# Kernel optimization log

Hardware: AMD Instinct MI355X
Metric: run time of the kernel (lower is better)

The kernel has to match this reference:

```python
import jax, jax.numpy as jnp
import numpy as np

N_NODES = 100000
N_EDGES = 1600000
HIDDEN = 128
EF_DIM = 16
LAYERS = 2
N_GRAPHS = 64


def _residual(x, W, b):
    # Residual(mlp_num=2): x + act(act(x@W0+b0)@W1+b1), act = silu
    h = jax.nn.silu(x @ W[0] + b[0])
    h = jax.nn.silu(h @ W[1] + b[1])
    return x + h


def setup_inputs() -> dict:
    key = jax.random.key(0)
    ks = jax.random.split(key, 10)
    scalar = jax.random.normal(ks[0], (N_NODES, HIDDEN), jnp.float32)
    ef = jax.random.normal(ks[1], (N_EDGES, EF_DIM), jnp.float32)
    edge_index = jax.random.randint(ks[2], (2, N_EDGES), 0, N_NODES, jnp.int32)
    C = jax.random.uniform(ks[3], (N_NODES, 1), dtype=jnp.float32)
    conv_smooth = jax.random.uniform(ks[4], (N_EDGES, 1), dtype=jnp.float32)
    batch_index = jnp.sort(jax.random.randint(ks[5], (N_NODES,), 0, N_GRAPHS, jnp.int32))
    # per VD_Conv layer: emb0, emb1, conv0, conv1, out0, out1 residual blocks; + 3 pooling blocks
    n_res = LAYERS * 6 + 3
    res_W = jax.random.normal(ks[6], (n_res, 2, HIDDEN, HIDDEN), jnp.float32) * 0.02
    res_b = jnp.zeros((n_res, 2, HIDDEN), jnp.float32)
    e_lin = jax.random.normal(ks[7], (LAYERS, EF_DIM, HIDDEN), jnp.float32) * 0.02
    return {"scalar": scalar, "ef": ef, "edge_index": edge_index, "C": C,
            "conv_smooth": conv_smooth, "batch_index": batch_index,
            "res_W": res_W, "res_b": res_b, "e_lin": e_lin}


def reference(scalar, ef, edge_index, C, conv_smooth, batch_index, res_W, res_b, e_lin):
    row, col = edge_index[0], edge_index[1]
    for i in range(LAYERS):
        p = 6 * i
        s_src = _residual(scalar, res_W[p], res_b[p])
        s_dst = _residual(scalar, res_W[p + 1], res_b[p + 1])
        conv_filter = (ef @ e_lin[i]) * conv_smooth            # [E, H]
        scalar_edge = s_dst[col] * conv_filter                 # gather + elementwise filter
        conv = jax.ops.segment_sum(scalar_edge, row, num_segments=N_NODES) * C  # scatter-reduce (agg='sum')
        conv = _residual(_residual(conv, res_W[p + 2], res_b[p + 2]), res_W[p + 3], res_b[p + 3])
        s = s_src * conv
        s = _residual(_residual(s, res_W[p + 4], res_b[p + 4]), res_W[p + 5], res_b[p + 5])
        scalar = s + scalar                                    # outer residual in Vanilla_DisGNN
    graph = jax.ops.segment_sum(scalar, batch_index, num_segments=N_GRAPHS)
    q = 6 * LAYERS
    for j in range(3):
        graph = _residual(graph, res_W[q + j], res_b[q + j])
    return graph
```

## Files before the change

### kernel.cpp

```cpp
#include <hip/hip_runtime.h>
#include <hip/hip_bf16.h>
#include <cstdint>
#include <cstddef>

#define HD 128
#define WOFF 16384

typedef __bf16    bf16x8 __attribute__((ext_vector_type(8)));
typedef float     f32x4  __attribute__((ext_vector_type(4)));
typedef _Float16  h2     __attribute__((ext_vector_type(2)));
typedef _Float16  h8     __attribute__((ext_vector_type(8)));

#if defined(__has_builtin)
#if __has_builtin(__builtin_amdgcn_fdot2)
#define HAVE_FDOT2 1
#endif
#endif

__device__ __forceinline__ float fdot2f(h2 a, h2 b, float c) {
#ifdef HAVE_FDOT2
    return __builtin_amdgcn_fdot2(a, b, c, false);
#else
    return c + (float)a[0]*(float)b[0] + (float)a[1]*(float)b[1];
#endif
}

__device__ __forceinline__ int swz(int r, int byteInRow) {
    int chunk = (byteInRow >> 4) ^ (r & 7);
    return r * 256 + (chunk << 4) + (byteInRow & 15);
}

__device__ __forceinline__ float silu_f(float v) { return v / (1.f + __expf(-v)); }


__device__ __forceinline__ void stage_x64(const float* __restrict__ x, char* lds,
                                          int r0, int nrows, int tid) {
    const int q = tid & 15;
    #pragma unroll
    for (int rr = 0; rr < 2; ++rr) {
        const int r  = (tid >> 4) + rr * 32;
        const int gr = r0 + r;
        float4 a = {0,0,0,0}, b = {0,0,0,0};
        if (gr < nrows) {
            const float4* p = (const float4*)(x + (size_t)gr * HD + q * 8);
            a = p[0]; b = p[1];
        }
        bf16x8 v;
        v[0]=(__bf16)a.x; v[1]=(__bf16)a.y; v[2]=(__bf16)a.z; v[3]=(__bf16)a.w;
        v[4]=(__bf16)b.x; v[5]=(__bf16)b.y; v[6]=(__bf16)b.z; v[7]=(__bf16)b.w;
        *(bf16x8*)(lds + swz(r, q * 16)) = v;
    }
}

__device__ __forceinline__ void load_wpref(const __bf16* __restrict__ w, bf16x8 pref[4], int tid) {
    #pragma unroll
    for (int i = 0; i < 4; ++i)
        pref[i] = *(const bf16x8*)(w + (size_t)(i * 512 + tid) * 8);
}
__device__ __forceinline__ void store_wpref(char* lds, const bf16x8 pref[4], int tid) {
    #pragma unroll
    for (int i = 0; i < 4; ++i) {
        const int l = i * 512 + tid;
        *(bf16x8*)(lds + WOFF + swz(l >> 4, (l & 15) * 16)) = pref[i];
    }
}

__device__ __forceinline__ void mm_pass_lds(const char* lds,
                                            const float* __restrict__ bias,
                                            int mrow0, int nbase, int crow, int kgrp, f32x4 acc[4]) {
    bf16x8 afr[4];
    #pragma unroll
    for (int kk = 0; kk < 4; ++kk)
        afr[kk] = *(const bf16x8*)(lds + swz(mrow0 + crow, kk*64 + kgrp*16));
    #pragma unroll
    for (int ni = 0; ni < 4; ++ni) {
        const float bv = bias[(nbase + ni) * 16 + crow];
        f32x4 t = {bv, bv, bv, bv};
        acc[ni] = t;
    }
    #pragma unroll
    for (int ni = 0; ni < 4; ++ni) {
        #pragma unroll
        for (int kk = 0; kk < 4; ++kk) {
            const bf16x8 bfr = *(const bf16x8*)(lds + WOFF + swz((nbase+ni)*16 + crow, kk*64 + kgrp*16));
            acc[ni] = __builtin_amdgcn_mfma_f32_16x16x32_bf16(afr[kk], bfr, acc[ni], 0, 0, 0);
        }
    }
}

__device__ __forceinline__ void write_h64(char* lds, const f32x4 acc[4],
                                          int mrow0, int nbase, int crow, int kgrp) {
    #pragma unroll
    for (int ni = 0; ni < 4; ++ni)
        #pragma unroll
        for (int rg = 0; rg < 4; ++rg)
            *(__bf16*)(lds + swz(mrow0 + kgrp*4 + rg, ((nbase+ni)*16 + crow)*2)) =
                (__bf16)silu_f(acc[ni][rg]);
}

__device__ __forceinline__ void restage64(char* lds, const f32x4 carry[4],
                                          int mrow0, int nbase, int crow, int kgrp) {
    #pragma unroll
    for (int ni = 0; ni < 4; ++ni)
        #pragma unroll
        for (int rg = 0; rg < 4; ++rg)
            *(__bf16*)(lds + swz(mrow0 + kgrp*4 + rg, ((nbase+ni)*16 + crow)*2)) =
                (__bf16)carry[ni][rg];
}

__global__ __launch_bounds__(512) void resid_dual_kernel(
    const float* __restrict__ x,
    const __bf16* __restrict__ wtA, const float* __restrict__ bA,
    const __bf16* __restrict__ wtB, const float* __restrict__ bB,
    __bf16* __restrict__ out1, __bf16* __restrict__ out2, int nrows)
{
    __shared__ char lds[49152];
    const int tid = threadIdx.x, lane = tid & 63, wv = tid >> 6;
    const int crow = lane & 15, kgrp = lane >> 4;
    const int r0 = blockIdx.x * 64;
    const int mrow0 = (wv >> 1) * 16, nbase = (wv & 1) * 4;

    {
        bf16x8 pref[4];
        load_wpref(wtA, pref, tid);
        stage_x64(x, lds, r0, nrows, tid);
        store_wpref(lds, pref, tid);
    }
    f32x4 acc[4], xe[4];
    #pragma unroll
    for (int ni = 0; ni < 4; ++ni)
        #pragma unroll
        for (int rg = 0; rg < 4; ++rg) {
            const int gr = r0 + mrow0 + kgrp*4 + rg;
            xe[ni][rg] = (gr < nrows) ? x[(size_t)gr*HD + (nbase+ni)*16 + crow] : 0.f;
        }
    __syncthreads();

    {
        bf16x8 pref[4];
        load_wpref(wtA + 16384, pref, tid);
        mm_pass_lds(lds, bA, mrow0, nbase, crow, kgrp, acc);
        __syncthreads();
        write_h64(lds, acc, mrow0, nbase, crow, kgrp);
        store_wpref(lds, pref, tid);
        __syncthreads();
    }
    {
        bf16x8 pref[4];
        load_wpref(wtB, pref, tid);
        mm_pass_lds(lds, bA + HD, mrow0, nbase, crow, kgrp, acc);
        #pragma unroll
        for (int ni = 0; ni < 4; ++ni)
            #pragma unroll
            for (int rg = 0; rg < 4; ++rg) {
                const int gr = r0 + mrow0 + kgrp*4 + rg;
                if (gr < nrows)
                    out1[(size_t)gr*HD + (nbase+ni)*16 + crow] =
                        (__bf16)(xe[ni][rg] + silu_f(acc[ni][rg]));
            }
        __syncthreads();
        restage64(lds, xe, mrow0, nbase, crow, kgrp);
        store_wpref(lds, pref, tid);
        __syncthreads();
    }
    {
        bf16x8 pref[4];
        load_wpref(wtB + 16384, pref, tid);
        mm_pass_lds(lds, bB, mrow0, nbase, crow, kgrp, acc);
        __syncthreads();
        write_h64(lds, acc, mrow0, nbase, crow, kgrp);
        store_wpref(lds, pref, tid);
        __syncthreads();
    }
    mm_pass_lds(lds, bB + HD, mrow0, nbase, crow, kgrp, acc);
    #pragma unroll
    for (int ni = 0; ni < 4; ++ni)
        #pragma unroll
        for (int rg = 0; rg < 4; ++rg) {
            const int gr = r0 + mrow0 + kgrp*4 + rg;
            if (gr < nrows)
                out2[(size_t)gr*HD + (nbase+ni)*16 + crow] =
                    (__bf16)(xe[ni][rg] + silu_f(acc[ni][rg]));
        }
}

__device__ __forceinline__ void sub_block(char* lds, const __bf16* __restrict__ w1,
                                          const __bf16* __restrict__ wNext0,
                                          const float* __restrict__ bias,
                                          int tid, int mrow0, int nbase, int crow, int kgrp,
                                          f32x4 carry[4], f32x4 acc[4]) {
    {
        bf16x8 pref[4];
        load_wpref(w1, pref, tid);
        mm_pass_lds(lds, bias, mrow0, nbase, crow, kgrp, acc);
        __syncthreads();
        write_h64(lds, acc, mrow0, nbase, crow, kgrp);
        store_wpref(lds, pref, tid);
        __syncthreads();
    }
    {
        bf16x8 pref[4];
        load_wpref(wNext0, pref, tid);
        mm_pass_lds(lds, bias + HD, mrow0, nbase, crow, kgrp, acc);
        #pragma unroll
        for (int ni = 0; ni < 4; ++ni)
            #pragma unroll
            for (int rg = 0; rg < 4; ++rg) carry[ni][rg] += silu_f(acc[ni][rg]);
        __syncthreads();
        restage64(lds, carry, mrow0, nbase, crow, kgrp);
        store_wpref(lds, pref, tid);
        __syncthreads();
    }
}

__global__ __launch_bounds__(512) void chain4_kernel(
    const float* __restrict__ x, const __bf16* __restrict__ mid,
    const __bf16* __restrict__ wA, const float* __restrict__ bA,
    const __bf16* __restrict__ wB, const float* __restrict__ bB,
    const __bf16* __restrict__ wC, const float* __restrict__ bC,
    const __bf16* __restrict__ wD, const float* __restrict__ bD,
    const float* __restrict__ post, float* __restrict__ y, int nrows)
{
    __shared__ char lds[49152];
    const int tid = threadIdx.x, lane = tid & 63, wv = tid >> 6;
    const int crow = lane & 15, kgrp = lane >> 4;
    const int r0 = blockIdx.x * 64;
    const int mrow0 = (wv >> 1) * 16, nbase = (wv & 1) * 4;

    {
        bf16x8 pref[4];
        load_wpref(wA, pref, tid);
        stage_x64(x, lds, r0, nrows, tid);
        store_wpref(lds, pref, tid);
    }
    f32x4 carry[4], acc[4];
    #pragma unroll
    for (int ni = 0; ni < 4; ++ni)
        #pragma unroll
        for (int rg = 0; rg < 4; ++rg) {
            const int gr = r0 + mrow0 + kgrp*4 + rg;
            carry[ni][rg] = (gr < nrows) ? x[(size_t)gr*HD + (nbase+ni)*16 + crow] : 0.f;
        }
    __syncthreads();

    sub_block(lds, wA + 16384, wB, bA, tid, mrow0, nbase, crow, kgrp, carry, acc);
    {
        bf16x8 pref[4];
        load_wpref(wB + 16384, pref, tid);
        mm_pass_lds(lds, bB, mrow0, nbase, crow, kgrp, acc);
        __syncthreads();
        write_h64(lds, acc, mrow0, nbase, crow, kgrp);
        store_wpref(lds, pref, tid);
        __syncthreads();
    }
    {
        bf16x8 pref[4];
        load_wpref(wC, pref, tid);
        mm_pass_lds(lds, bB + HD, mrow0, nbase, crow, kgrp, acc);
        #pragma unroll
        for (int ni = 0; ni < 4; ++ni)
            #pragma unroll
            for (int rg = 0; rg < 4; ++rg) {
                const int gr = r0 + mrow0 + kgrp*4 + rg;
                const float m = (gr < nrows) ? (float)mid[(size_t)gr*HD + (nbase+ni)*16 + crow] : 0.f;
                carry[ni][rg] = (carry[ni][rg] + silu_f(acc[ni][rg])) * m;
            }
        __syncthreads();
        restage64(lds, carry, mrow0, nbase, crow, kgrp);
        store_wpref(lds, pref, tid);
        __syncthreads();
    }
    sub_block(lds, wC + 16384, wD, bC, tid, mrow0, nbase, crow, kgrp, carry, acc);
    {
        bf16x8 pref[4];
        load_wpref(wD + 16384, pref, tid);
        mm_pass_lds(lds, bD, mrow0, nbase, crow, kgrp, acc);
        __syncthreads();
        write_h64(lds, acc, mrow0, nbase, crow, kgrp);
        store_wpref(lds, pref, tid);
        __syncthreads();
    }
    mm_pass_lds(lds, bD + HD, mrow0, nbase, crow, kgrp, acc);
    #pragma unroll
    for (int ni = 0; ni < 4; ++ni)
        #pragma unroll
        for (int rg = 0; rg < 4; ++rg) {
            const int gr = r0 + mrow0 + kgrp*4 + rg;
            if (gr < nrows) {
                const int cc = (nbase+ni)*16 + crow;
                y[(size_t)gr*HD + cc] = carry[ni][rg] + silu_f(acc[ni][rg]) + post[(size_t)gr*HD + cc];
            }
        }
}

__global__ __launch_bounds__(512) void chain3_kernel(
    const float* __restrict__ x,
    const __bf16* __restrict__ wA, const float* __restrict__ bA,
    const __bf16* __restrict__ wB, const float* __restrict__ bB,
    const __bf16* __restrict__ wC, const float* __restrict__ bC,
    float* __restrict__ y, int nrows)
{
    __shared__ char lds[49152];
    const int tid = threadIdx.x, lane = tid & 63, wv = tid >> 6;
    const int crow = lane & 15, kgrp = lane >> 4;
    const int r0 = blockIdx.x * 64;
    const int mrow0 = (wv >> 1) * 16, nbase = (wv & 1) * 4;

    {
        bf16x8 pref[4];
        load_wpref(wA, pref, tid);
        stage_x64(x, lds, r0, nrows, tid);
        store_wpref(lds, pref, tid);
    }
    f32x4 carry[4], acc[4];
    #pragma unroll
    for (int ni = 0; ni < 4; ++ni)
        #pragma unroll
        for (int rg = 0; rg < 4; ++rg) {
            const int gr = r0 + mrow0 + kgrp*4 + rg;
            carry[ni][rg] = (gr < nrows) ? x[(size_t)gr*HD + (nbase+ni)*16 + crow] : 0.f;
        }
    __syncthreads();

    sub_block(lds, wA + 16384, wB, bA, tid, mrow0, nbase, crow, kgrp, carry, acc);
    sub_block(lds, wB + 16384, wC, bB, tid, mrow0, nbase, crow, kgrp, carry, acc);
    {
        bf16x8 pref[4];
        load_wpref(wC + 16384, pref, tid);
        mm_pass_lds(lds, bC, mrow0, nbase, crow, kgrp, acc);
        __syncthreads();
        write_h64(lds, acc, mrow0, nbase, crow, kgrp);
        store_wpref(lds, pref, tid);
        __syncthreads();
    }
    mm_pass_lds(lds, bC + HD, mrow0, nbase, crow, kgrp, acc);
    #pragma unroll
    for (int ni = 0; ni < 4; ++ni)
        #pragma unroll
        for (int rg = 0; rg < 4; ++rg) {
            const int gr = r0 + mrow0 + kgrp*4 + rg;
            if (gr < nrows)
                y[(size_t)gr*HD + (nbase+ni)*16 + crow] = carry[ni][rg] + silu_f(acc[ni][rg]);
        }
}

__global__ __launch_bounds__(256) void hist_kernel(const int* __restrict__ erow, int* __restrict__ cnt, int E) {
    int i = blockIdx.x * blockDim.x + threadIdx.x;
    const int stride = gridDim.x * blockDim.x;
    for (; i < E; i += stride) atomicAdd(&cnt[erow[i]], 1);
}

__global__ __launch_bounds__(256) void scan1_kernel(const int* __restrict__ cnt, int* __restrict__ part, int n) {
    __shared__ int red[256];
    const int base = blockIdx.x * 1024;
    int s = 0;
    for (int i = threadIdx.x; i < 1024; i += 256) {
        const int idx = base + i;
        s += (idx < n) ? cnt[idx] : 0;
    }
    red[threadIdx.x] = s; __syncthreads();
    for (int o = 128; o > 0; o >>= 1) {
        if (threadIdx.x < o) red[threadIdx.x] += red[threadIdx.x + o];
        __syncthreads();
    }
    if (threadIdx.x == 0) part[blockIdx.x] = red[0];
}

__global__ __launch_bounds__(256) void scan2_kernel(int* __restrict__ part, int nb,
                                                    int* __restrict__ rowptr, int n) {
    __shared__ int sh[257];
    const int tid = threadIdx.x;
    int a[4]; int s = 0;
    #pragma unroll
    for (int q = 0; q < 4; ++q) {
        const int i = tid*4 + q;
        a[q] = (i < nb) ? part[i] : 0;
        s += a[q];
    }
    sh[tid + 1] = s; __syncthreads();
    if (tid == 0) {
        sh[0] = 0;
        int run = 0;
        for (int i = 1; i <= 256; ++i) { run += sh[i]; sh[i] = run; }
    }
    __syncthreads();
    int off = sh[tid];
    #pragma unroll
    for (int q = 0; q < 4; ++q) {
        const int i = tid*4 + q;
        if (i < nb) part[i] = off;
        off += a[q];
    }
    if (tid == 255) rowptr[n] = off;
}

__global__ __launch_bounds__(256) void scan3_kernel(const int* __restrict__ cnt, const int* __restrict__ part,
                                                    int* __restrict__ rowptr, int n) {
    __shared__ int sc[257];
    const int base = blockIdx.x * 1024;
    const int i0 = base + threadIdx.x * 4;
    int v[4]; int s = 0;
    #pragma unroll
    for (int q = 0; q < 4; ++q) {
        const int idx = i0 + q;
        v[q] = (idx < n) ? cnt[idx] : 0;
        s += v[q];
    }
    sc[threadIdx.x + 1] = s; __syncthreads();
    if (threadIdx.x == 0) {
        int run = 0;
        for (int i = 0; i < 256; ++i) { const int t = sc[i + 1]; sc[i + 1] = run; run += t; }
    }
    __syncthreads();
    int off = part[blockIdx.x] + sc[threadIdx.x + 1];
    #pragma unroll
    for (int q = 0; q < 4; ++q) {
        const int idx = i0 + q;
        if (idx < n) rowptr[idx] = off;
        off += v[q];
    }
}

__global__ __launch_bounds__(256) void scatter_reorder_kernel(
    const int* __restrict__ erow, const int* __restrict__ ecol,
    const float* __restrict__ ef, const float* __restrict__ cs,
    const int* __restrict__ rowptr, int* __restrict__ cursor,
    int* __restrict__ csr_col, _Float16* __restrict__ csr_ef, int E)
{
    int i = blockIdx.x * blockDim.x + threadIdx.x;
    const int stride = gridDim.x * blockDim.x;
    for (; i < E; i += stride) {
        const int r = erow[i];
        const int p = rowptr[r] + atomicAdd(&cursor[r], 1);
        csr_col[p] = ecol[i];
        const float c = cs[i];
        const float4* ep = (const float4*)(ef + (size_t)i * 16);
        const float4 e0 = ep[0], e1 = ep[1], e2 = ep[2], e3 = ep[3];
        h8 v0, v1;
        v0[0]=(_Float16)(e0.x*c); v0[1]=(_Float16)(e0.y*c); v0[2]=(_Float16)(e0.z*c); v0[3]=(_Float16)(e0.w*c);
        v0[4]=(_Float16)(e1.x*c); v0[5]=(_Float16)(e1.y*c); v0[6]=(_Float16)(e1.z*c); v0[7]=(_Float16)(e1.w*c);
        v1[0]=(_Float16)(e2.x*c); v1[1]=(_Float16)(e2.y*c); v1[2]=(_Float16)(e2.z*c); v1[3]=(_Float16)(e2.w*c);
        v1[4]=(_Float16)(e3.x*c); v1[5]=(_Float16)(e3.y*c); v1[6]=(_Float16)(e3.z*c); v1[7]=(_Float16)(e3.w*c);
        h8* dst = (h8*)(csr_ef + (size_t)p * 16);
        dst[0] = v0; dst[1] = v1;
    }
}

__global__ __launch_bounds__(256) void elin16_kernel(const float* __restrict__ elin,
                                                     _Float16* __restrict__ out, int total) {
    const int i = blockIdx.x * 256 + threadIdx.x;
    if (i < total) out[i] = (_Float16)elin[i];
}

__device__ __forceinline__ float bfu_lo(uint32_t u) { return __uint_as_float(u << 16); }
__device__ __forceinline__ float bfu_hi(uint32_t u) { return __uint_as_float(u & 0xffff0000u); }

__device__ __forceinline__ void edge_dot(const h8 a0, const h8 a1,
                                         const h2 w0[8], const h2 w1[8],
                                         float& f0, float& f1) {
    #pragma unroll
    for (int kk = 0; kk < 4; ++kk) {
        h2 p = {a0[2*kk], a0[2*kk+1]};
        f0 = fdot2f(p, w0[kk], f0);
        f1 = fdot2f(p, w1[kk], f1);
    }
    #pragma unroll
    for (int kk = 0; kk < 4; ++kk) {
        h2 p = {a1[2*kk], a1[2*kk+1]};
        f0 = fdot2f(p, w0[4+kk], f0);
        f1 = fdot2f(p, w1[4+kk], f1);
    }
}

__global__ __launch_bounds__(256) void conv_kernel(
    const _Float16* __restrict__ csr_ef, const int* __restrict__ csr_col,
    const _Float16* __restrict__ elin16, const int* __restrict__ rowptr,
    const __bf16* __restrict__ sdst, const float* __restrict__ Cn,
    float* __restrict__ conv, int nnodes)
{
    const int wv   = __builtin_amdgcn_readfirstlane(threadIdx.x >> 6);
    const int lane = threadIdx.x & 63;
    const int v = blockIdx.x * 4 + wv;
    if (v >= nnodes) return;
    const int j0 = lane * 2;

    h2 w0[8], w1[8];
    #pragma unroll
    for (int kk = 0; kk < 8; ++kk) {
        w0[kk][0] = elin16[(2*kk)   * HD + j0];
        w0[kk][1] = elin16[(2*kk+1) * HD + j0];
        w1[kk][0] = elin16[(2*kk)   * HD + j0 + 1];
        w1[kk][1] = elin16[(2*kk+1) * HD + j0 + 1];
    }

    const uint16_t* sd = (const uint16_t*)sdst;
    const int beg = rowptr[v], end = rowptr[v + 1];
    float acc0 = 0.f, acc1 = 0.f;
    int t = beg;
    for (; t + 8 <= end; t += 8) {
        int c[8];
        #pragma unroll
        for (int q = 0; q < 8; ++q) c[q] = csr_col[t + q];
        uint32_t u[8];
        #pragma unroll
        for (int q = 0; q < 8; ++q)
            u[q] = *(const uint32_t*)(sd + (size_t)c[q] * HD + j0);
        #pragma unroll
        for (int q = 0; q < 8; ++q) {
            const h8* ep = (const h8*)(csr_ef + (size_t)(t + q) * 16);
            const h8 a0 = ep[0], a1 = ep[1];
            float f0 = 0.f, f1 = 0.f;
            edge_dot(a0, a1, w0, w1, f0, f1);
            acc0 = fmaf(bfu_lo(u[q]), f0, acc0);
            acc1 = fmaf(bfu_hi(u[q]), f1, acc1);
        }
    }
    for (; t + 2 <= end; t += 2) {
        int c[2];
        c[0] = csr_col[t]; c[1] = csr_col[t + 1];
        uint32_t u[2];
        u[0] = *(const uint32_t*)(sd + (size_t)c[0] * HD + j0);
        u[1] = *(const uint32_t*)(sd + (size_t)c[1] * HD + j0);
        #pragma unroll
        for (int q = 0; q < 2; ++q) {
            const h8* ep = (const h8*)(csr_ef + (size_t)(t + q) * 16);
            const h8 a0 = ep[0], a1 = ep[1];
            float f0 = 0.f, f1 = 0.f;
            edge_dot(a0, a1, w0, w1, f0, f1);
            acc0 = fmaf(bfu_lo(u[q]), f0, acc0);
            acc1 = fmaf(bfu_hi(u[q]), f1, acc1);
        }
    }
    if (t < end) {
        const int c = csr_col[t];
        const uint32_t u = *(const uint32_t*)(sd + (size_t)c * HD + j0);
        const h8* ep = (const h8*)(csr_ef + (size_t)t * 16);
        const h8 a0 = ep[0], a1 = ep[1];
        float f0 = 0.f, f1 = 0.f;
        edge_dot(a0, a1, w0, w1, f0, f1);
        acc0 = fmaf(bfu_lo(u), f0, acc0);
        acc1 = fmaf(bfu_hi(u), f1, acc1);
    }
    const float cn = Cn[v];
    float2 out = {acc0 * cn, acc1 * cn};
    *(float2*)(conv + (size_t)v * HD + j0) = out;
}

__global__ __launch_bounds__(256) void pool_kernel(
    const float* __restrict__ s, const int* __restrict__ bidx,
    float* __restrict__ g, int n)
{
    const int slot = threadIdx.x >> 5;
    const int jc   = (threadIdx.x & 31) * 4;
    const int base = blockIdx.x * 256;
    if (base >= n) return;
    const int end = (base + 256 < n) ? base + 256 : n;
    float4 acc = {0,0,0,0};
    int cur = -1;
    for (int i = base + slot; i < end; i += 8) {
        const int b = bidx[i];
        if (b != cur) {
            if (cur >= 0) {
                atomicAdd(g + (size_t)cur*HD + jc + 0, acc.x);
                atomicAdd(g + (size_t)cur*HD + jc + 1, acc.y);
                atomicAdd(g + (size_t)cur*HD + jc + 2, acc.z);
                atomicAdd(g + (size_t)cur*HD + jc + 3, acc.w);
            }
            acc = {0,0,0,0};
            cur = b;
        }
        const float4 v = *(const float4*)(s + (size_t)i*HD + jc);
        acc.x += v.x; acc.y += v.y; acc.z += v.z; acc.w += v.w;
    }
    if (cur >= 0) {
        atomicAdd(g + (size_t)cur*HD + jc + 0, acc.x);
        atomicAdd(g + (size_t)cur*HD + jc + 1, acc.y);
        atomicAdd(g + (size_t)cur*HD + jc + 2, acc.z);
        atomicAdd(g + (size_t)cur*HD + jc + 3, acc.w);
    }
}

__global__ __launch_bounds__(256) void convw_kernel(const float* __restrict__ W, __bf16* __restrict__ wt, int total) {
    const int idx = blockIdx.x * 256 + threadIdx.x;
    if (idx >= total) return;
    const int mat = idx >> 14;
    const int rem = idx & 16383;
    const int jj = rem >> 7, kk = rem & 127;
    wt[idx] = (__bf16)W[(size_t)mat * 16384 + kk * HD + jj];
}

extern "C" void kernel_launch(void* const* d_in, const int* in_sizes, int n_in,
                              void* d_out, int out_size, void* d_ws, size_t ws_size,
                              hipStream_t stream) {
    const float* scalar = (const float*)d_in[0];
    const float* ef     = (const float*)d_in[1];
    const int*   eidx   = (const int*)  d_in[2];
    const float* Cn     = (const float*)d_in[3];
    const float* cs     = (const float*)d_in[4];
    const int*   bidx   = (const int*)  d_in[5];
    const float* resW   = (const float*)d_in[6];
    const float* resB   = (const float*)d_in[7];
    const float* elin   = (const float*)d_in[8];

    const int N      = in_sizes[0] / HD;
    const int E      = in_sizes[1] / 16;
    const int n_res  = in_sizes[7] / (2 * HD);
    const int layers = (n_res - 3) / 6;
    const int G      = out_size / HD;
    const size_t nfeat = (size_t)N * HD;

    char* p = (char*)d_ws;
    auto alloc = [&](size_t bytes) { char* q = p; p += (bytes + 255) & ~(size_t)255; return q; };
    float*    A      = (float*)alloc(nfeat * 4);
    float*    Dc     = (float*)alloc(nfeat * 4);
    __bf16*   Bs16   = (__bf16*)alloc(nfeat * 2);
    __bf16*   Cs16   = (__bf16*)alloc(nfeat * 2);
    __bf16*   wt     = (__bf16*)alloc((size_t)n_res * 2 * 16384 * 2);
    float*    graph  = (float*)alloc((size_t)G * HD * 4);
    int*      rowptr = (int*)alloc((size_t)(N + 1) * 4);
    int*      rowcnt = (int*)alloc((size_t)N * 4);
    int*      csr_col= (int*)alloc((size_t)E * 4);
    _Float16* csr_ef = (_Float16*)alloc((size_t)E * 16 * 2);
    _Float16* elin16 = (_Float16*)alloc((size_t)layers * 16 * HD * 2);
    int*      part   = (int*)alloc(1024 * 4);

    const int* erow = eidx;
    const int* ecol = eidx + E;

    const int totW = n_res * 2 * 16384;
    convw_kernel<<<(totW + 255) / 256, 256, 0, stream>>>(resW, wt, totW);
    const int totE = layers * 16 * HD;
    elin16_kernel<<<(totE + 255) / 256, 256, 0, stream>>>(elin, elin16, totE);

    const int nchunks = (N + 1023) / 1024;
    hipMemsetAsync(rowcnt, 0, (size_t)N * 4, stream);
    hist_kernel<<<1024, 256, 0, stream>>>(erow, rowcnt, E);
    scan1_kernel<<<nchunks, 256, 0, stream>>>(rowcnt, part, N);
    scan2_kernel<<<1, 256, 0, stream>>>(part, nchunks, rowptr, N);
    scan3_kernel<<<nchunks, 256, 0, stream>>>(rowcnt, part, rowptr, N);
    hipMemsetAsync(rowcnt, 0, (size_t)N * 4, stream);
    scatter_reorder_kernel<<<1024, 256, 0, stream>>>(erow, ecol, ef, cs, rowptr, rowcnt, csr_col, csr_ef, E);

    const int gridR = (N + 63) / 64;
    const float* cur = scalar;
    for (int i = 0; i < layers; ++i) {
        const int pb = 6 * i;
        resid_dual_kernel<<<gridR, 512, 0, stream>>>(
            cur,
            wt + (size_t)pb * 32768, resB + (size_t)pb * 256,
            wt + (size_t)(pb + 1) * 32768, resB + (size_t)(pb + 1) * 256,
            Bs16, Cs16, N);
        conv_kernel<<<(N + 3) / 4, 256, 0, stream>>>(
            csr_ef, csr_col, elin16 + (size_t)i * 16 * HD, rowptr, Cs16, Cn, Dc, N);
        chain4_kernel<<<gridR, 512, 0, stream>>>(
            Dc, Bs16,
            wt + (size_t)(pb + 2) * 32768, resB + (size_t)(pb + 2) * 256,
            wt + (size_t)(pb + 3) * 32768, resB + (size_t)(pb + 3) * 256,
            wt + (size_t)(pb + 4) * 32768, resB + (size_t)(pb + 4) * 256,
            wt + (size_t)(pb + 5) * 32768, resB + (size_t)(pb + 5) * 256,
            cur, A, N);
        cur = A;
    }

    hipMemsetAsync(graph, 0, (size_t)G * HD * 4, stream);
    pool_kernel<<<(N + 255) / 256, 256, 0, stream>>>(cur, bidx, graph, N);

    const int q = 6 * layers;
    const int gridG = (G + 63) / 64;
    chain3_kernel<<<gridG, 512, 0, stream>>>(
        graph,
        wt + (size_t)q * 32768, resB + (size_t)q * 256,
        wt + (size_t)(q + 1) * 32768, resB + (size_t)(q + 1) * 256,
        wt + (size_t)(q + 2) * 32768, resB + (size_t)(q + 2) * 256,
        (float*)d_out, G);
}
```

Measured before the change: 840.9 us.

## Switch residual MLP kernels to 32x32 MFMA tiles with direct global-to-LDS weight staging

```diff
diff --git a/kernel.cpp b/kernel.cpp
--- a/kernel.cpp
+++ b/kernel.cpp
@@ -8,8 +8,12 @@
 
 typedef __bf16    bf16x8 __attribute__((ext_vector_type(8)));
 typedef float     f32x4  __attribute__((ext_vector_type(4)));
+typedef float     f32x16 __attribute__((ext_vector_type(16)));
 typedef _Float16  h2     __attribute__((ext_vector_type(2)));
 typedef _Float16  h8     __attribute__((ext_vector_type(8)));
+
+typedef __attribute__((address_space(1))) const unsigned char ga_u8;
+typedef __attribute__((address_space(3))) unsigned char lds_u8;
 
 #if defined(__has_builtin)
 #if __has_builtin(__builtin_amdgcn_fdot2)
@@ -32,6 +36,23 @@
 
 __device__ __forceinline__ float silu_f(float v) { return v / (1.f + __expf(-v)); }
 
+__device__ __forceinline__ int crow32(int r, int lane) {
+    return (r & 3) + 8 * (r >> 2) + 4 * (lane >> 5);
+}
+
+
+__device__ __forceinline__ void issue_wstage(const __bf16* __restrict__ w, char* lds, int tid) {
+    const int wv = tid >> 6, lane = tid & 63;
+    const char* g = (const char*)w;
+    #pragma unroll
+    for (int i = 0; i < 4; ++i) {
+        const int seg = (wv << 2) | i;
+        __builtin_amdgcn_global_load_lds(
+            (ga_u8*)(g + seg * 1024 + lane * 16),
+            (lds_u8*)(lds + WOFF + seg * 1024),
+            16, 0, 0);
+    }
+}
 
 __device__ __forceinline__ void stage_x64(const float* __restrict__ x, char* lds,
                                           int r0, int nrows, int tid) {
@@ -52,60 +73,43 @@
     }
 }
 
-__device__ __forceinline__ void load_wpref(const __bf16* __restrict__ w, bf16x8 pref[4], int tid) {
-    #pragma unroll
-    for (int i = 0; i < 4; ++i)
-        pref[i] = *(const bf16x8*)(w + (size_t)(i * 512 + tid) * 8);
-}
-__device__ __forceinline__ void store_wpref(char* lds, const bf16x8 pref[4], int tid) {
-    #pragma unroll
-    for (int i = 0; i < 4; ++i) {
-        const int l = i * 512 + tid;
-        *(bf16x8*)(lds + WOFF + swz(l >> 4, (l & 15) * 16)) = pref[i];
-    }
-}
-
-__device__ __forceinline__ void mm_pass_lds(const char* lds,
-                                            const float* __restrict__ bias,
-                                            int mrow0, int nbase, int crow, int kgrp, f32x4 acc[4]) {
-    bf16x8 afr[4];
-    #pragma unroll
-    for (int kk = 0; kk < 4; ++kk)
-        afr[kk] = *(const bf16x8*)(lds + swz(mrow0 + crow, kk*64 + kgrp*16));
-    #pragma unroll
-    for (int ni = 0; ni < 4; ++ni) {
-        const float bv = bias[(nbase + ni) * 16 + crow];
-        f32x4 t = {bv, bv, bv, bv};
-        acc[ni] = t;
-    }
-    #pragma unroll
-    for (int ni = 0; ni < 4; ++ni) {
-        #pragma unroll
-        for (int kk = 0; kk < 4; ++kk) {
-            const bf16x8 bfr = *(const bf16x8*)(lds + WOFF + swz((nbase+ni)*16 + crow, kk*64 + kgrp*16));
-            acc[ni] = __builtin_amdgcn_mfma_f32_16x16x32_bf16(afr[kk], bfr, acc[ni], 0, 0, 0);
-        }
-    }
-}
-
-__device__ __forceinline__ void write_h64(char* lds, const f32x4 acc[4],
-                                          int mrow0, int nbase, int crow, int kgrp) {
-    #pragma unroll
-    for (int ni = 0; ni < 4; ++ni)
-        #pragma unroll
-        for (int rg = 0; rg < 4; ++rg)
-            *(__bf16*)(lds + swz(mrow0 + kgrp*4 + rg, ((nbase+ni)*16 + crow)*2)) =
-                (__bf16)silu_f(acc[ni][rg]);
-}
-
-__device__ __forceinline__ void restage64(char* lds, const f32x4 carry[4],
-                                          int mrow0, int nbase, int crow, int kgrp) {
-    #pragma unroll
-    for (int ni = 0; ni < 4; ++ni)
-        #pragma unroll
-        for (int rg = 0; rg < 4; ++rg)
-            *(__bf16*)(lds + swz(mrow0 + kgrp*4 + rg, ((nbase+ni)*16 + crow)*2)) =
-                (__bf16)carry[ni][rg];
+__device__ __forceinline__ void mm_pass32(const char* lds, const float* __restrict__ bias,
+                                          int rowtile, int coltile, int lane,
+                                          f32x16& accA, f32x16& accB) {
+    const int rowA = rowtile * 32 + (lane & 31);
+    const int rowB = coltile * 32 + (lane & 31);
+    const int kb   = (lane >> 5) * 16;
+    bf16x8 afr[8];
+    #pragma unroll
+    for (int s = 0; s < 8; ++s)
+        afr[s] = *(const bf16x8*)(lds + swz(rowA, s * 32 + kb));
+    const float bv = bias[coltile * 32 + (lane & 31)];
+    #pragma unroll
+    for (int r = 0; r < 16; ++r) { accA[r] = bv; accB[r] = 0.f; }
+    #pragma unroll
+    for (int s = 0; s < 8; s += 2) {
+        const bf16x8 b0 = *(const bf16x8*)(lds + WOFF + swz(rowB, s * 32 + kb));
+        accA = __builtin_amdgcn_mfma_f32_32x32x16_bf16(afr[s], b0, accA, 0, 0, 0);
+        const bf16x8 b1 = *(const bf16x8*)(lds + WOFF + swz(rowB, (s + 1) * 32 + kb));
+        accB = __builtin_amdgcn_mfma_f32_32x32x16_bf16(afr[s + 1], b1, accB, 0, 0, 0);
+    }
+}
+
+__device__ __forceinline__ void write_h32(char* lds, const f32x16& aA, const f32x16& aB,
+                                          int rowtile, int coltile, int lane) {
+    const int colb = (coltile * 32 + (lane & 31)) * 2;
+    #pragma unroll
+    for (int r = 0; r < 16; ++r)
+        *(__bf16*)(lds + swz(rowtile * 32 + crow32(r, lane), colb)) =
+            (__bf16)silu_f(aA[r] + aB[r]);
+}
+
+__device__ __forceinline__ void restage32(char* lds, const float carry[16],
+                                          int rowtile, int coltile, int lane) {
+    const int colb = (coltile * 32 + (lane & 31)) * 2;
+    #pragma unroll
+    for (int r = 0; r < 16; ++r)
+        *(__bf16*)(lds + swz(rowtile * 32 + crow32(r, lane), colb)) = (__bf16)carry[r];
 }
 
 __global__ __launch_bounds__(512) void resid_dual_kernel(
@@ -116,100 +120,48 @@
 {
     __shared__ char lds[49152];
     const int tid = threadIdx.x, lane = tid & 63, wv = tid >> 6;
-    const int crow = lane & 15, kgrp = lane >> 4;
+    const int rowtile = wv >> 2, coltile = wv & 3;
     const int r0 = blockIdx.x * 64;
-    const int mrow0 = (wv >> 1) * 16, nbase = (wv & 1) * 4;
-
-    {
-        bf16x8 pref[4];
-        load_wpref(wtA, pref, tid);
-        stage_x64(x, lds, r0, nrows, tid);
-        store_wpref(lds, pref, tid);
-    }
-    f32x4 acc[4], xe[4];
-    #pragma unroll
-    for (int ni = 0; ni < 4; ++ni)
-        #pragma unroll
-        for (int rg = 0; rg < 4; ++rg) {
-            const int gr = r0 + mrow0 + kgrp*4 + rg;
-            xe[ni][rg] = (gr < nrows) ? x[(size_t)gr*HD + (nbase+ni)*16 + crow] : 0.f;
-        }
-    __syncthreads();
-
-    {
-        bf16x8 pref[4];
-        load_wpref(wtA + 16384, pref, tid);
-        mm_pass_lds(lds, bA, mrow0, nbase, crow, kgrp, acc);
-        __syncthreads();
-        write_h64(lds, acc, mrow0, nbase, crow, kgrp);
-        store_wpref(lds, pref, tid);
-        __syncthreads();
-    }
-    {
-        bf16x8 pref[4];
-        load_wpref(wtB, pref, tid);
-        mm_pass_lds(lds, bA + HD, mrow0, nbase, crow, kgrp, acc);
-        #pragma unroll
-        for (int ni = 0; ni < 4; ++ni)
-            #pragma unroll
-            for (int rg = 0; rg < 4; ++rg) {
-                const int gr = r0 + mrow0 + kgrp*4 + rg;
-                if (gr < nrows)
-                    out1[(size_t)gr*HD + (nbase+ni)*16 + crow] =
-                        (__bf16)(xe[ni][rg] + silu_f(acc[ni][rg]));
-            }
-        __syncthreads();
-        restage64(lds, xe, mrow0, nbase, crow, kgrp);
-        store_wpref(lds, pref, tid);
-        __syncthreads();
-    }
-    {
-        bf16x8 pref[4];
-        load_wpref(wtB + 16384, pref, tid);
-        mm_pass_lds(lds, bB, mrow0, nbase, crow, kgrp, acc);
-        __syncthreads();
-        write_h64(lds, acc, mrow0, nbase, crow, kgrp);
-        store_wpref(lds, pref, tid);
-        __syncthreads();
-    }
-    mm_pass_lds(lds, bB + HD, mrow0, nbase, crow, kgrp, acc);
-    #pragma unroll
-    for (int ni = 0; ni < 4; ++ni)
-        #pragma unroll
-        for (int rg = 0; rg < 4; ++rg) {
-            const int gr = r0 + mrow0 + kgrp*4 + rg;
-            if (gr < nrows)
-                out2[(size_t)gr*HD + (nbase+ni)*16 + crow] =
-                    (__bf16)(xe[ni][rg] + silu_f(acc[ni][rg]));
-        }
-}
-
-__device__ __forceinline__ void sub_block(char* lds, const __bf16* __restrict__ w1,
-                                          const __bf16* __restrict__ wNext0,
-                                          const float* __restrict__ bias,
-                                          int tid, int mrow0, int nbase, int crow, int kgrp,
-                                          f32x4 carry[4], f32x4 acc[4]) {
-    {
-        bf16x8 pref[4];
-        load_wpref(w1, pref, tid);
-        mm_pass_lds(lds, bias, mrow0, nbase, crow, kgrp, acc);
-        __syncthreads();
-        write_h64(lds, acc, mrow0, nbase, crow, kgrp);
-        store_wpref(lds, pref, tid);
-        __syncthreads();
-    }
-    {
-        bf16x8 pref[4];
-        load_wpref(wNext0, pref, tid);
-        mm_pass_lds(lds, bias + HD, mrow0, nbase, crow, kgrp, acc);
-        #pragma unroll
-        for (int ni = 0; ni < 4; ++ni)
-            #pragma unroll
-            for (int rg = 0; rg < 4; ++rg) carry[ni][rg] += silu_f(acc[ni][rg]);
-        __syncthreads();
-        restage64(lds, carry, mrow0, nbase, crow, kgrp);
-        store_wpref(lds, pref, tid);
-        __syncthreads();
+    const int colg = coltile * 32 + (lane & 31);
+
+    issue_wstage(wtA, lds, tid);
+    stage_x64(x, lds, r0, nrows, tid);
+    f32x16 accA, accB;
+    float xe[16];
+    #pragma unroll
+    for (int r = 0; r < 16; ++r) {
+        const int gr = r0 + rowtile * 32 + crow32(r, lane);
+        xe[r] = (gr < nrows) ? x[(size_t)gr * HD + colg] : 0.f;
+    }
+    __syncthreads();
+
+    mm_pass32(lds, bA, rowtile, coltile, lane, accA, accB);
+    __syncthreads();
+    issue_wstage(wtA + 16384, lds, tid);
+    write_h32(lds, accA, accB, rowtile, coltile, lane);
+    __syncthreads();
+    mm_pass32(lds, bA + HD, rowtile, coltile, lane, accA, accB);
+    #pragma unroll
+    for (int r = 0; r < 16; ++r) {
+        const int gr = r0 + rowtile * 32 + crow32(r, lane);
+        if (gr < nrows)
+            out1[(size_t)gr * HD + colg] = (__bf16)(xe[r] + silu_f(accA[r] + accB[r]));
+    }
+    __syncthreads();
+    issue_wstage(wtB, lds, tid);
+    restage32(lds, xe, rowtile, coltile, lane);
+    __syncthreads();
+    mm_pass32(lds, bB, rowtile, coltile, lane, accA, accB);
+    __syncthreads();
+    issue_wstage(wtB + 16384, lds, tid);
+    write_h32(lds, accA, accB, rowtile, coltile, lane);
+    __syncthreads();
+    mm_pass32(lds, bB + HD, rowtile, coltile, lane, accA, accB);
+    #pragma unroll
+    for (int r = 0; r < 16; ++r) {
+        const int gr = r0 + rowtile * 32 + crow32(r, lane);
+        if (gr < nrows)
+            out2[(size_t)gr * HD + colg] = (__bf16)(xe[r] + silu_f(accA[r] + accB[r]));
     }
 }
 
@@ -223,74 +175,74 @@
 {
     __shared__ char lds[49152];
     const int tid = threadIdx.x, lane = tid & 63, wv = tid >> 6;
-    const int crow = lane & 15, kgrp = lane >> 4;
+    const int rowtile = wv >> 2, coltile = wv & 3;
     const int r0 = blockIdx.x * 64;
-    const int mrow0 = (wv >> 1) * 16, nbase = (wv & 1) * 4;
-
-    {
-        bf16x8 pref[4];
-        load_wpref(wA, pref, tid);
-        stage_x64(x, lds, r0, nrows, tid);
-        store_wpref(lds, pref, tid);
-    }
-    f32x4 carry[4], acc[4];
-    #pragma unroll
-    for (int ni = 0; ni < 4; ++ni)
-        #pragma unroll
-        for (int rg = 0; rg < 4; ++rg) {
-            const int gr = r0 + mrow0 + kgrp*4 + rg;
-            carry[ni][rg] = (gr < nrows) ? x[(size_t)gr*HD + (nbase+ni)*16 + crow] : 0.f;
-        }
-    __syncthreads();
-
-    sub_block(lds, wA + 16384, wB, bA, tid, mrow0, nbase, crow, kgrp, carry, acc);
-    {
-        bf16x8 pref[4];
-        load_wpref(wB + 16384, pref, tid);
-        mm_pass_lds(lds, bB, mrow0, nbase, crow, kgrp, acc);
-        __syncthreads();
-        write_h64(lds, acc, mrow0, nbase, crow, kgrp);
-        store_wpref(lds, pref, tid);
-        __syncthreads();
-    }
-    {
-        bf16x8 pref[4];
-        load_wpref(wC, pref, tid);
-        mm_pass_lds(lds, bB + HD, mrow0, nbase, crow, kgrp, acc);
-        #pragma unroll
-        for (int ni = 0; ni < 4; ++ni)
-            #pragma unroll
-            for (int rg = 0; rg < 4; ++rg) {
-                const int gr = r0 + mrow0 + kgrp*4 + rg;
-                const float m = (gr < nrows) ? (float)mid[(size_t)gr*HD + (nbase+ni)*16 + crow] : 0.f;
-                carry[ni][rg] = (carry[ni][rg] + silu_f(acc[ni][rg])) * m;
-            }
-        __syncthreads();
-        restage64(lds, carry, mrow0, nbase, crow, kgrp);
-        store_wpref(lds, pref, tid);
-        __syncthreads();
-    }
-    sub_block(lds, wC + 16384, wD, bC, tid, mrow0, nbase, crow, kgrp, carry, acc);
-    {
-        bf16x8 pref[4];
-        load_wpref(wD + 16384, pref, tid);
-        mm_pass_lds(lds, bD, mrow0, nbase, crow, kgrp, acc);
-        __syncthreads();
-        write_h64(lds, acc, mrow0, nbase, crow, kgrp);
-        store_wpref(lds, pref, tid);
-        __syncthreads();
-    }
-    mm_pass_lds(lds, bD + HD, mrow0, nbase, crow, kgrp, acc);
-    #pragma unroll
-    for (int ni = 0; ni < 4; ++ni)
-        #pragma unroll
-        for (int rg = 0; rg < 4; ++rg) {
-            const int gr = r0 + mrow0 + kgrp*4 + rg;
-            if (gr < nrows) {
-                const int cc = (nbase+ni)*16 + crow;
-                y[(size_t)gr*HD + cc] = carry[ni][rg] + silu_f(acc[ni][rg]) + post[(size_t)gr*HD + cc];
-            }
-        }
+    const int colg = coltile * 32 + (lane & 31);
+
+    issue_wstage(wA, lds, tid);
+    stage_x64(x, lds, r0, nrows, tid);
+    f32x16 accA, accB;
+    float carry[16];
+    #pragma unroll
+    for (int r = 0; r < 16; ++r) {
+        const int gr = r0 + rowtile * 32 + crow32(r, lane);
+        carry[r] = (gr < nrows) ? x[(size_t)gr * HD + colg] : 0.f;
+    }
+    __syncthreads();
+
+    mm_pass32(lds, bA, rowtile, coltile, lane, accA, accB);
+    __syncthreads();
+    issue_wstage(wA + 16384, lds, tid);
+    write_h32(lds, accA, accB, rowtile, coltile, lane);
+    __syncthreads();
+    mm_pass32(lds, bA + HD, rowtile, coltile, lane, accA, accB);
+    #pragma unroll
+    for (int r = 0; r < 16; ++r) carry[r] += silu_f(accA[r] + accB[r]);
+    __syncthreads();
+    issue_wstage(wB, lds, tid);
+    restage32(lds, carry, rowtile, coltile, lane);
+    __syncthreads();
+    mm_pass32(lds, bB, rowtile, coltile, lane, accA, accB);
+    __syncthreads();
+    issue_wstage(wB + 16384, lds, tid);
+    write_h32(lds, accA, accB, rowtile, coltile, lane);
+    __syncthreads();
+    mm_pass32(lds, bB + HD, rowtile, coltile, lane, accA, accB);
+    #pragma unroll
+    for (int r = 0; r < 16; ++r) {
+        const int gr = r0 + rowtile * 32 + crow32(r, lane);
+        const float m = (gr < nrows) ? (float)mid[(size_t)gr * HD + colg] : 0.f;
+        carry[r] = (carry[r] + silu_f(accA[r] + accB[r])) * m;
+    }
+    __syncthreads();
+    issue_wstage(wC, lds, tid);
+    restage32(lds, carry, rowtile, coltile, lane);
+    __syncthreads();
+    mm_pass32(lds, bC, rowtile, coltile, lane, accA, accB);
+    __syncthreads();
+    issue_wstage(wC + 16384, lds, tid);
+    write_h32(lds, accA, accB, rowtile, coltile, lane);
+    __syncthreads();
+    mm_pass32(lds, bC + HD, rowtile, coltile, lane, accA, accB);
+    #pragma unroll
+    for (int r = 0; r < 16; ++r) carry[r] += silu_f(accA[r] + accB[r]);
+    __syncthreads();
+    issue_wstage(wD, lds, tid);
+    restage32(lds, carry, rowtile, coltile, lane);
+    __syncthreads();
+    mm_pass32(lds, bD, rowtile, coltile, lane, accA, accB);
+    __syncthreads();
+    issue_wstage(wD + 16384, lds, tid);
+    write_h32(lds, accA, accB, rowtile, coltile, lane);
+    __syncthreads();
+    mm_pass32(lds, bD + HD, rowtile, coltile, lane, accA, accB);
+    #pragma unroll
+    for (int r = 0; r < 16; ++r) {
+        const int gr = r0 + rowtile * 32 + crow32(r, lane);
+        if (gr < nrows)
+            y[(size_t)gr * HD + colg] =
+                carry[r] + silu_f(accA[r] + accB[r]) + post[(size_t)gr * HD + colg];
+    }
 }
 
 __global__ __launch_bounds__(512) void chain3_kernel(
@@ -302,46 +254,47 @@
 {
     __shared__ char lds[49152];
     const int tid = threadIdx.x, lane = tid & 63, wv = tid >> 6;
-    const int crow = lane & 15, kgrp = lane >> 4;
+    const int rowtile = wv >> 2, coltile = wv & 3;
     const int r0 = blockIdx.x * 64;
-    const int mrow0 = (wv >> 1) * 16, nbase = (wv & 1) * 4;
-
-    {
-        bf16x8 pref[4];
-        load_wpref(wA, pref, tid);
-        stage_x64(x, lds, r0, nrows, tid);
-        store_wpref(lds, pref, tid);
-    }
-    f32x4 carry[4], acc[4];
-    #pragma unroll
-    for (int ni = 0; ni < 4; ++ni)
+    const int colg = coltile * 32 + (lane & 31);
+
+    issue_wstage(wA, lds, tid);
+    stage_x64(x, lds, r0, nrows, tid);
+    f32x16 accA, accB;
+    float carry[16];
+    #pragma unroll
+    for (int r = 0; r < 16; ++r) {
+        const int gr = r0 + rowtile * 32 + crow32(r, lane);
+        carry[r] = (gr < nrows) ? x[(size_t)gr * HD + colg] : 0.f;
+    }
+    __syncthreads();
+
+    const __bf16* w1s[3] = {wA + 16384, wB + 16384, wC + 16384};
+    const __bf16* w0next[3] = {wB, wC, nullptr};
+    const float* bs[3] = {bA, bB, bC};
+    #pragma unroll
+    for (int sb = 0; sb < 3; ++sb) {
+        mm_pass32(lds, bs[sb], rowtile, coltile, lane, accA, accB);
+        __syncthreads();
+        issue_wstage(w1s[sb], lds, tid);
+        write_h32(lds, accA, accB, rowtile, coltile, lane);
+        __syncthreads();
+        mm_pass32(lds, bs[sb] + HD, rowtile, coltile, lane, accA, accB);
         #pragma unroll
-        for (int rg = 0; rg < 4; ++rg) {
-            const int gr = r0 + mrow0 + kgrp*4 + rg;
-            carry[ni][rg] = (gr < nrows) ? x[(size_t)gr*HD + (nbase+ni)*16 + crow] : 0.f;
+        for (int r = 0; r < 16; ++r) carry[r] += silu_f(accA[r] + accB[r]);
+        if (sb < 2) {
+            __syncthreads();
+            issue_wstage(w0next[sb], lds, tid);
+            restage32(lds, carry, rowtile, coltile, lane);
+            __syncthreads();
         }
-    __syncthreads();
-
-    sub_block(lds, wA + 16384, wB, bA, tid, mrow0, nbase, crow, kgrp, carry, acc);
-    sub_block(lds, wB + 16384, wC, bB, tid, mrow0, nbase, crow, kgrp, carry, acc);
-    {
-        bf16x8 pref[4];
-        load_wpref(wC + 16384, pref, tid);
-        mm_pass_lds(lds, bC, mrow0, nbase, crow, kgrp, acc);
-        __syncthreads();
-        write_h64(lds, acc, mrow0, nbase, crow, kgrp);
-        store_wpref(lds, pref, tid);
-        __syncthreads();
-    }
-    mm_pass_lds(lds, bC + HD, mrow0, nbase, crow, kgrp, acc);
-    #pragma unroll
-    for (int ni = 0; ni < 4; ++ni)
-        #pragma unroll
-        for (int rg = 0; rg < 4; ++rg) {
-            const int gr = r0 + mrow0 + kgrp*4 + rg;
-            if (gr < nrows)
-                y[(size_t)gr*HD + (nbase+ni)*16 + crow] = carry[ni][rg] + silu_f(acc[ni][rg]);
-        }
+    }
+    #pragma unroll
+    for (int r = 0; r < 16; ++r) {
+        const int gr = r0 + rowtile * 32 + crow32(r, lane);
+        if (gr < nrows)
+            y[(size_t)gr * HD + colg] = carry[r];
+    }
 }
 
 __global__ __launch_bounds__(256) void hist_kernel(const int* __restrict__ erow, int* __restrict__ cnt, int E) {
@@ -585,8 +538,11 @@
     if (idx >= total) return;
     const int mat = idx >> 14;
     const int rem = idx & 16383;
-    const int jj = rem >> 7, kk = rem & 127;
-    wt[idx] = (__bf16)W[(size_t)mat * 16384 + kk * HD + jj];
+    const int j = rem >> 7;
+    const int b = rem & 127;
+    const int c = b >> 3, e = b & 7;
+    const int k = ((c ^ (j & 7)) << 3) | e;
+    wt[idx] = (__bf16)W[(size_t)mat * 16384 + k * HD + j];
 }
 
 extern "C" void kernel_launch(void* const* d_in, const int* in_sizes, int n_in,
```

New measurement: 876.0 us. +4.2%, slower.
